# Optimization experiments

Measured on AMD Instinct MI355X. Metric: run time of the kernel, lower is better.

## Reference

```python
import jax, jax.numpy as jnp
import numpy as np


def setup_inputs() -> dict:
    key = jax.random.key(0)
    k1, k2, k3, k4 = jax.random.split(key, 4)
    S, D = 16384, 2048  # seq_len, 2*hidden_size
    outputs = jax.random.normal(k1, (S, D), dtype=jnp.float32)
    W = jax.random.normal(k2, (D, D), dtype=jnp.float32) * (1.0 / np.sqrt(D))
    b = jax.random.normal(k3, (D,), dtype=jnp.float32) * 0.01
    weight_vec = jax.random.normal(k4, (D,), dtype=jnp.float32) * (1.0 / np.sqrt(D))
    return {"outputs": outputs, "W": W, "b": b, "weight_vec": weight_vec}


def reference(outputs, W, b, weight_vec):
    # Original: per-timestep energy_i = dot(v, Linear(outputs[i])) in a Python loop.
    # Fused: one GEMM over all timesteps, then a matvec, then softmax over seq.
    energy = jnp.einsum('sd,ed->se', outputs, W) + b      # [S, D] (Linear: x @ W^T + b)
    attn_energies = jnp.einsum('se,e->s', energy, weight_vec)  # [S]
    attn = jax.nn.softmax(attn_energies, axis=0)
    return attn[None, None, :]  # [1, 1, S]
```

## Files before the change

### kernel.cpp

```cpp
#include <hip/hip_runtime.h>

#define SEQ 16384
#define DIM 2048


__global__ __launch_bounds__(256) void k_compute_u(const float* __restrict__ W,
                                                   const float* __restrict__ v,
                                                   float* __restrict__ u) {
    const int d  = blockIdx.x * 256 + threadIdx.x;
    const int e0 = blockIdx.y * 64;
    float acc = 0.f;
#pragma unroll 8
    for (int i = 0; i < 64; ++i) {
        const int e = e0 + i;
        acc = fmaf(W[(size_t)e * DIM + d], v[e], acc);
    }
    atomicAdd(&u[d], acc);
}

__global__ __launch_bounds__(256) void k_energies_fused(const float* __restrict__ O,
                                                        const float* __restrict__ u,
                                                        float* __restrict__ expE,
                                                        float* __restrict__ S_part) {
    const int tid  = threadIdx.x;
    const int lane = tid & 63;
    const int wid  = tid >> 6;
    __shared__ float ps[4];

    const float4* __restrict__ up = (const float4*)u;
    float4 uw[8];
#pragma unroll
    for (int it = 0; it < 8; ++it) uw[it] = up[it * 64 + lane];

    const int row0 = blockIdx.x * 16 + wid * 4;
    float pw = 0.f;
#pragma unroll
    for (int r = 0; r < 4; ++r) {
        const int row = row0 + r;
        const float4* __restrict__ rowp = (const float4*)(O + (size_t)row * DIM);
        float acc = 0.f;
#pragma unroll
        for (int it = 0; it < 8; ++it) {
            const float4 x = rowp[it * 64 + lane];
            const float4 w = uw[it];
            acc = fmaf(x.x, w.x, fmaf(x.y, w.y, fmaf(x.z, w.z, fmaf(x.w, w.w, acc))));
        }
#pragma unroll
        for (int off = 32; off > 0; off >>= 1) acc += __shfl_down(acc, off, 64);
        if (lane == 0) {
            const float p = __expf(acc);
            expE[row] = p;
            pw += p;
        }
    }
    if (lane == 0) ps[wid] = pw;
    __syncthreads();
    if (tid == 0) atomicAdd(&S_part[blockIdx.x & 7], ps[0] + ps[1] + ps[2] + ps[3]);
}

__global__ __launch_bounds__(256) void k_normalize(const float* __restrict__ expE,
                                                   const float* __restrict__ S_part,
                                                   float* __restrict__ out) {
    __shared__ float invS;
    if (threadIdx.x == 0) {
        float s = 0.f;
#pragma unroll
        for (int i = 0; i < 8; ++i) s += S_part[i];
        invS = 1.0f / s;
    }
    __syncthreads();
    const int i = blockIdx.x * 256 + threadIdx.x;
    out[i] = expE[i] * invS;
}

extern "C" void kernel_launch(void* const* d_in, const int* in_sizes, int n_in,
                              void* d_out, int out_size, void* d_ws, size_t ws_size,
                              hipStream_t stream) {
    const float* outputs    = (const float*)d_in[0];
    const float* W          = (const float*)d_in[1];
    const float* weight_vec = (const float*)d_in[3];
    float* out = (float*)d_out;

    float* S_part = (float*)d_ws;
    float* u      = S_part + 8;
    float* expE   = S_part + 2064;

    hipMemsetAsync(d_ws, 0, (8 + DIM) * sizeof(float), stream);

    dim3 gU(DIM / 256, 32);
    k_compute_u<<<gU, 256, 0, stream>>>(W, weight_vec, u);

    k_energies_fused<<<SEQ / 16, 256, 0, stream>>>(outputs, u, expE, S_part);

    k_normalize<<<SEQ / 256, 256, 0, stream>>>(expE, S_part, out);
}
```

Measured before the change: 211.3 us.

## Fuse all stages into one cooperative kernel with grid syncs

```diff
diff --git a/kernel.cpp b/kernel.cpp
--- a/kernel.cpp
+++ b/kernel.cpp
@@ -1,8 +1,118 @@
 #include <hip/hip_runtime.h>
+#include <hip/hip_cooperative_groups.h>
 
 #define SEQ 16384
 #define DIM 2048
-
+#define NTHR 256
+#define NBLK 512
+#define NGRP 1024
+#define ESPLIT 128
+#define ECHUNK (DIM / ESPLIT)
+
+namespace cg = cooperative_groups;
+
+
+__global__ __launch_bounds__(NTHR, 2) void k_fused(const float* __restrict__ O,
+                                                   const float* __restrict__ W,
+                                                   const float* __restrict__ v,
+                                                   float* __restrict__ ws,
+                                                   float* __restrict__ out) {
+    float* part   = ws;
+    float* u      = part + ESPLIT * DIM;
+    float* expE   = u + DIM;
+    float* blkSum = expE + SEQ;
+
+    const int tid  = threadIdx.x;
+    const int bid  = blockIdx.x;
+    const int lane = tid & 63;
+    const int wid  = tid >> 6;
+
+    cg::grid_group grid = cg::this_grid();
+
+#pragma unroll
+    for (int gi = 0; gi < NGRP / NBLK; ++gi) {
+        const int unit = bid + gi * NBLK;
+        const int db = unit & 7;
+        const int es = unit >> 3;
+        const int d  = db * NTHR + tid;
+        float acc = 0.f;
+#pragma unroll
+        for (int i = 0; i < ECHUNK; ++i) {
+            const int e = es * ECHUNK + i;
+            acc = fmaf(W[(size_t)e * DIM + d], v[e], acc);
+        }
+        part[es * DIM + d] = acc;
+    }
+    grid.sync();
+
+    if (bid < 8) {
+        const int d = bid * NTHR + tid;
+        float s = 0.f;
+        for (int es = 0; es < ESPLIT; ++es) s += part[es * DIM + d];
+        u[d] = s;
+    }
+    grid.sync();
+
+    {
+        __shared__ float ps[4];
+        const float4* __restrict__ up = (const float4*)u;
+        float4 uw[8];
+#pragma unroll
+        for (int it = 0; it < 8; ++it) uw[it] = up[it * 64 + lane];
+
+#pragma unroll
+        for (int gi = 0; gi < NGRP / NBLK; ++gi) {
+            const int g    = bid + gi * NBLK;
+            const int row0 = g * 16 + wid * 4;
+            float pw = 0.f;
+#pragma unroll
+            for (int r = 0; r < 4; ++r) {
+                const int row = row0 + r;
+                const float4* __restrict__ rowp = (const float4*)(O + (size_t)row * DIM);
+                float acc = 0.f;
+#pragma unroll
+                for (int it = 0; it < 8; ++it) {
+                    const float4 x = rowp[it * 64 + lane];
+                    const float4 w = uw[it];
+                    acc = fmaf(x.x, w.x, fmaf(x.y, w.y, fmaf(x.z, w.z, fmaf(x.w, w.w, acc))));
+                }
+#pragma unroll
+                for (int off = 32; off > 0; off >>= 1) acc += __shfl_down(acc, off, 64);
+                if (lane == 0) {
+                    const float p = __expf(acc);
+                    expE[row] = p;
+                    pw += p;
+                }
+            }
+            if (lane == 0) ps[wid] = pw;
+            __syncthreads();
+            if (tid == 0) blkSum[g] = ps[0] + ps[1] + ps[2] + ps[3];
+            __syncthreads();
+        }
+    }
+    grid.sync();
+
+    {
+        __shared__ float red[4];
+        float s = 0.f;
+#pragma unroll
+        for (int i = 0; i < 4; ++i) s += blkSum[tid * 4 + i];
+#pragma unroll
+        for (int off = 32; off > 0; off >>= 1) s += __shfl_down(s, off, 64);
+        if (lane == 0) red[wid] = s;
+        __syncthreads();
+        const float invS = 1.0f / (red[0] + red[1] + red[2] + red[3]);
+        if (tid < 16) {
+#pragma unroll
+            for (int gi = 0; gi < NGRP / NBLK; ++gi) {
+                const int i = (bid + gi * NBLK) * 16 + tid;
+                out[i] = expE[i] * invS;
+            }
+        }
+    }
+}
+
+#define FB_OFF (1 << 21)
 
 __global__ __launch_bounds__(256) void k_compute_u(const float* __restrict__ W,
                                                    const float* __restrict__ v,
@@ -76,21 +186,23 @@
 extern "C" void kernel_launch(void* const* d_in, const int* in_sizes, int n_in,
                               void* d_out, int out_size, void* d_ws, size_t ws_size,
                               hipStream_t stream) {
-    const float* outputs    = (const float*)d_in[0];
-    const float* W          = (const float*)d_in[1];
-    const float* weight_vec = (const float*)d_in[3];
+    const float* O = (const float*)d_in[0];
+    const float* W = (const float*)d_in[1];
+    const float* v = (const float*)d_in[3];
     float* out = (float*)d_out;
-
-    float* S_part = (float*)d_ws;
-    float* u      = S_part + 8;
-    float* expE   = S_part + 2064;
-
-    hipMemsetAsync(d_ws, 0, (8 + DIM) * sizeof(float), stream);
-
-    dim3 gU(DIM / 256, 32);
-    k_compute_u<<<gU, 256, 0, stream>>>(W, weight_vec, u);
-
-    k_energies_fused<<<SEQ / 16, 256, 0, stream>>>(outputs, u, expE, S_part);
-
-    k_normalize<<<SEQ / 256, 256, 0, stream>>>(expE, S_part, out);
-}
+    float* ws  = (float*)d_ws;
+
+    void* args[] = {(void*)&O, (void*)&W, (void*)&v, (void*)&ws, (void*)&out};
+    hipError_t err = hipLaunchCooperativeKernel((void*)k_fused, dim3(NBLK),
+                                                dim3(NTHR), args, 0, stream);
+    if (err != hipSuccess) {
+        float* S_part = ws + FB_OFF;
+        float* u      = S_part + 8;
+        float* expE   = S_part + 2064;
+        hipMemsetAsync(S_part, 0, (8 + DIM) * sizeof(float), stream);
+        dim3 gU(DIM / 256, 32);
+        k_compute_u<<<gU, 256, 0, stream>>>(W, v, u);
+        k_energies_fused<<<SEQ / 16, 256, 0, stream>>>(O, u, expE, S_part);
+        k_normalize<<<SEQ / 256, 256, 0, stream>>>(expE, S_part, out);
+    }
+}
```

Result: slower. 370.7 us (+75.4%).

## Replace atomics and memset with deterministic two-stage reductions, smaller energy blocks

Applied to the files above, without the earlier changes.

```diff
diff --git a/kernel.cpp b/kernel.cpp
--- a/kernel.cpp
+++ b/kernel.cpp
@@ -4,24 +4,34 @@
 #define DIM 2048
 
 
-__global__ __launch_bounds__(256) void k_compute_u(const float* __restrict__ W,
-                                                   const float* __restrict__ v,
-                                                   float* __restrict__ u) {
+__global__ __launch_bounds__(256) void k_wtv_part(const float* __restrict__ W,
+                                                  const float* __restrict__ v,
+                                                  float* __restrict__ part) {
     const int d  = blockIdx.x * 256 + threadIdx.x;
-    const int e0 = blockIdx.y * 64;
+    const int es = blockIdx.y;
+    const int e0 = es * 64;
     float acc = 0.f;
 #pragma unroll 8
     for (int i = 0; i < 64; ++i) {
         const int e = e0 + i;
         acc = fmaf(W[(size_t)e * DIM + d], v[e], acc);
     }
-    atomicAdd(&u[d], acc);
+    part[es * DIM + d] = acc;
 }
 
-__global__ __launch_bounds__(256) void k_energies_fused(const float* __restrict__ O,
-                                                        const float* __restrict__ u,
-                                                        float* __restrict__ expE,
-                                                        float* __restrict__ S_part) {
+__global__ __launch_bounds__(256) void k_wtv_reduce(const float* __restrict__ part,
+                                                    float* __restrict__ u) {
+    const int d = blockIdx.x * 256 + threadIdx.x;
+    float s = 0.f;
+#pragma unroll
+    for (int es = 0; es < 32; ++es) s += part[es * DIM + d];
+    u[d] = s;
+}
+
+__global__ __launch_bounds__(256) void k_energies(const float* __restrict__ O,
+                                                  const float* __restrict__ u,
+                                                  float* __restrict__ expE,
+                                                  float* __restrict__ blkSum) {
     const int tid  = threadIdx.x;
     const int lane = tid & 63;
     const int wid  = tid >> 6;
@@ -32,65 +42,72 @@
 #pragma unroll
     for (int it = 0; it < 8; ++it) uw[it] = up[it * 64 + lane];
 
-    const int row0 = blockIdx.x * 16 + wid * 4;
-    float pw = 0.f;
+    const int row0 = blockIdx.x * 8 + wid * 2;
+    const float4* __restrict__ rp0 = (const float4*)(O + (size_t)row0 * DIM);
+    const float4* __restrict__ rp1 = (const float4*)(O + (size_t)(row0 + 1) * DIM);
+
+    float acc0 = 0.f, acc1 = 0.f;
 #pragma unroll
-    for (int r = 0; r < 4; ++r) {
-        const int row = row0 + r;
-        const float4* __restrict__ rowp = (const float4*)(O + (size_t)row * DIM);
-        float acc = 0.f;
+    for (int it = 0; it < 8; ++it) {
+        const float4 x = rp0[it * 64 + lane];
+        const float4 y = rp1[it * 64 + lane];
+        const float4 w = uw[it];
+        acc0 = fmaf(x.x, w.x, fmaf(x.y, w.y, fmaf(x.z, w.z, fmaf(x.w, w.w, acc0))));
+        acc1 = fmaf(y.x, w.x, fmaf(y.y, w.y, fmaf(y.z, w.z, fmaf(y.w, w.w, acc1))));
+    }
 #pragma unroll
-        for (int it = 0; it < 8; ++it) {
-            const float4 x = rowp[it * 64 + lane];
-            const float4 w = uw[it];
-            acc = fmaf(x.x, w.x, fmaf(x.y, w.y, fmaf(x.z, w.z, fmaf(x.w, w.w, acc))));
-        }
-#pragma unroll
-        for (int off = 32; off > 0; off >>= 1) acc += __shfl_down(acc, off, 64);
-        if (lane == 0) {
-            const float p = __expf(acc);
-            expE[row] = p;
-            pw += p;
-        }
+    for (int off = 32; off > 0; off >>= 1) {
+        acc0 += __shfl_down(acc0, off, 64);
+        acc1 += __shfl_down(acc1, off, 64);
     }
-    if (lane == 0) ps[wid] = pw;
+    if (lane == 0) {
+        const float p0 = __expf(acc0);
+        const float p1 = __expf(acc1);
+        expE[row0]     = p0;
+        expE[row0 + 1] = p1;
+        ps[wid] = p0 + p1;
+    }
     __syncthreads();
-    if (tid == 0) atomicAdd(&S_part[blockIdx.x & 7], ps[0] + ps[1] + ps[2] + ps[3]);
+    if (tid == 0) blkSum[blockIdx.x] = ps[0] + ps[1] + ps[2] + ps[3];
 }
 
-__global__ __launch_bounds__(256) void k_normalize(const float* __restrict__ expE,
-                                                   const float* __restrict__ S_part,
-                                                   float* __restrict__ out) {
-    __shared__ float invS;
-    if (threadIdx.x == 0) {
-        float s = 0.f;
+__global__ __launch_bounds__(256) void k_finish(const float* __restrict__ expE,
+                                                const float* __restrict__ blkSum,
+                                                float* __restrict__ out) {
+    const int tid  = threadIdx.x;
+    const int lane = tid & 63;
+    const int wid  = tid >> 6;
+    __shared__ float red[4];
+
+    float s = 0.f;
 #pragma unroll
-        for (int i = 0; i < 8; ++i) s += S_part[i];
-        invS = 1.0f / s;
-    }
+    for (int i = 0; i < 8; ++i) s += blkSum[tid * 8 + i];
+#pragma unroll
+    for (int off = 32; off > 0; off >>= 1) s += __shfl_down(s, off, 64);
+    if (lane == 0) red[wid] = s;
     __syncthreads();
-    const int i = blockIdx.x * 256 + threadIdx.x;
+    const float invS = 1.0f / (red[0] + red[1] + red[2] + red[3]);
+
+    const int i = blockIdx.x * 256 + tid;
     out[i] = expE[i] * invS;
 }
 
 extern "C" void kernel_launch(void* const* d_in, const int* in_sizes, int n_in,
                               void* d_out, int out_size, void* d_ws, size_t ws_size,
                               hipStream_t stream) {
-    const float* outputs    = (const float*)d_in[0];
-    const float* W          = (const float*)d_in[1];
-    const float* weight_vec = (const float*)d_in[3];
+    const float* O = (const float*)d_in[0];
+    const float* W = (const float*)d_in[1];
+    const float* v = (const float*)d_in[3];
     float* out = (float*)d_out;
 
-    float* S_part = (float*)d_ws;
-    float* u      = S_part + 8;
-    float* expE   = S_part + 2064;
+    float* part   = (float*)d_ws;
+    float* u      = part + 32 * DIM;
+    float* expE   = u + DIM;
+    float* blkSum = expE + SEQ;
 
-    hipMemsetAsync(d_ws, 0, (8 + DIM) * sizeof(float), stream);
-
-    dim3 gU(DIM / 256, 32);
-    k_compute_u<<<gU, 256, 0, stream>>>(W, weight_vec, u);
-
-    k_energies_fused<<<SEQ / 16, 256, 0, stream>>>(outputs, u, expE, S_part);
-
-    k_normalize<<<SEQ / 256, 256, 0, stream>>>(expE, S_part, out);
+    dim3 g1(DIM / 256, 32);
+    k_wtv_part<<<g1, 256, 0, stream>>>(W, v, part);
+    k_wtv_reduce<<<DIM / 256, 256, 0, stream>>>(part, u);
+    k_energies<<<SEQ / 8, 256, 0, stream>>>(O, u, expE, blkSum);
+    k_finish<<<SEQ / 256, 256, 0, stream>>>(expE, blkSum, out);
 }
```

Measured after the change: 210.8 us. No clear change (-0.2%).
